# Optimization experiments

Measured on AMD Instinct MI355X. Metric: run time of the kernel, lower is better.

The kernel has to match this reference:

```python
import jax, jax.numpy as jnp
import numpy as np

N_HEAD = 16
ROPE_CACHE = 2500  # Rotary module caches tables of length 2500
NEG_INF = -1e30


def _rope_tables(head_dim):
    inv_freq = 1.0 / (10000.0 ** (jnp.arange(0, head_dim, 2, dtype=jnp.float32) / head_dim))
    t = jnp.arange(ROPE_CACHE, dtype=jnp.float32)
    freqs = t[:, None] * inv_freq[None, :]            # (2500, head_dim//2)
    emb = jnp.concatenate([freqs, freqs], axis=-1)    # (2500, head_dim)
    return jnp.cos(emb), jnp.sin(emb)


def _rotate_half(x):
    h = x.shape[-1] // 2
    return jnp.concatenate([-x[..., h:], x[..., :h]], axis=-1)


def setup_inputs() -> dict:
    key = jax.random.key(0)
    ks = jax.random.split(key, 8)
    B, S, D = 2, 2048, 1024
    H = N_HEAD
    hd = D // H
    return {
        "qx": jax.random.normal(ks[0], (B, S, D), jnp.float32),
        "kvx": jax.random.normal(ks[1], (B, S, D), jnp.float32),
        "k_cache": jnp.zeros((B, H, S, hd), jnp.float32),
        "v_cache": jnp.zeros((B, H, S, hd), jnp.float32),
        "Wq": jax.random.normal(ks[2], (D, D), jnp.float32) * 0.02,
        "bq": jnp.zeros((D,), jnp.float32),
        "Wk": jax.random.normal(ks[3], (D, D), jnp.float32) * 0.02,
        "Wv": jax.random.normal(ks[4], (D, D), jnp.float32) * 0.02,
        "bv": jnp.zeros((D,), jnp.float32),
        "Wo": jax.random.normal(ks[5], (D, D), jnp.float32) * 0.02,
        "bo": jnp.zeros((D,), jnp.float32),
        "q_positions": jnp.arange(S, dtype=jnp.int32),
        "kv_positions": jnp.arange(S, dtype=jnp.int32),
    }


def reference(qx, kvx, k_cache, v_cache, Wq, bq, Wk, Wv, bv, Wo, bo, q_positions, kv_positions):
    B, Sq, D = qx.shape
    H = N_HEAD
    hd = D // H
    Skv = kvx.shape[1]
    cos, sin = _rope_tables(hd)
    # sqrt_qk_scale = sqrt(1) = 1, folded out.

    def rope(x, pos):  # x: (B, S, H, hd)
        c = cos[pos][None, :, None, :]
        s = sin[pos][None, :, None, :]
        return x * c + _rotate_half(x) * s

    # projections (torch Linear: y = x @ W.T + b; key has no bias)
    q = (qx @ Wq.T + bq).reshape(B, Sq, H, hd)
    q = rope(q, q_positions).transpose(0, 2, 1, 3)            # (B,H,Sq,hd)
    k = (kvx @ Wk.T).reshape(B, Skv, H, hd)
    k = rope(k, kv_positions).transpose(0, 2, 1, 3)           # (B,H,Skv,hd)
    v = (kvx @ Wv.T + bv).reshape(B, Skv, H, hd).transpose(0, 2, 1, 3)

    # KV-cache scatter update: k_cache[:, :, kv_positions] = k
    k_cache = k_cache.at[:, :, kv_positions].set(k)
    v_cache = v_cache.at[:, :, kv_positions].set(v)
    Sc = k_cache.shape[2]

    # SDPA (causal), scaled by 1/sqrt(head_dim) as in F.scaled_dot_product_attention
    scores = jnp.einsum('bhqd,bhkd->bhqk', q, k_cache) / jnp.sqrt(jnp.float32(hd))
    causal = jnp.arange(Sq)[:, None] >= jnp.arange(Sc)[None, :]
    scores = jnp.where(causal[None, None], scores, NEG_INF)
    attn = jax.nn.softmax(scores, axis=-1)
    wv = jnp.einsum('bhqk,bhkd->bhqd', attn, v_cache)

    out = wv.transpose(0, 2, 1, 3).reshape(B, Sq, D) @ Wo.T + bo
    return out
```

## Files before the change

kernel.cpp:

```cpp
#include <hip/hip_runtime.h>
#include <cstdint>
#include <cstddef>

#define NH   16
#define SEQ  2048
#define DM   1024
#define HD   64
#define KDIM 1024
#define MROWS 4096
#define CH   2

using short8  = __attribute__((ext_vector_type(8))) short;
using short4v = __attribute__((ext_vector_type(4))) short;
using floatx4 = __attribute__((ext_vector_type(4))) float;

__device__ __forceinline__ short f2bf(float f) {
  unsigned int u = __float_as_uint(f);
  u += 0x7fffu + ((u >> 16) & 1u);
  return (short)(u >> 16);
}
__device__ __forceinline__ float bf2f(short s) {
  return __uint_as_float(((unsigned int)(unsigned short)s) << 16);
}

__device__ __forceinline__ void async_ld16(const void* g, void* l) {
  __builtin_amdgcn_global_load_lds(
      (const __attribute__((address_space(1))) void*)g,
      (__attribute__((address_space(3))) void*)l, 16, 0, 0);
}

struct Cvt8 {
  const float* src[8];
  void* dst[8];
  int n[8];
  const int* pos[8];
};

__global__ void convert8(Cvt8 a) {
  const int which = blockIdx.y;
  const int stride = gridDim.x * blockDim.x;
  if (which < 6) {
    const float4* s = (const float4*)a.src[which];
    short4v* d = (short4v*)a.dst[which];
    const int n4 = a.n[which] >> 2;
    for (int i = blockIdx.x * blockDim.x + threadIdx.x; i < n4; i += stride) {
      float4 v = s[i];
      short4v o;
      o.x = f2bf(v.x); o.y = f2bf(v.y); o.z = f2bf(v.z); o.w = f2bf(v.w);
      d[i] = o;
    }
  } else {
    const int* pos = a.pos[which];
    float2* d = (float2*)a.dst[which];
    const int n = a.n[which];
    for (int i = blockIdx.x * blockDim.x + threadIdx.x; i < n; i += stride) {
      int s = i >> 5, d1 = i & 31;
      float fr = __powf(10000.f, -(float)d1 * (1.f / 32.f));
      float ang = (float)pos[s] * fr;
      float sn, cs;
      __sincosf(ang, &sn, &cs);
      d[i] = make_float2(cs, sn);
    }
  }
}

__device__ __forceinline__ void gemm_core(const short* __restrict__ A,
                                          const short* __restrict__ B,
                                          int row0, int col0,
                                          short* As, short* Bs,
                                          floatx4 (&acc)[4][4], int tid) {
  const int lane = tid & 63;
  const int w = tid >> 6;
  const int quad = lane >> 4;
  const int ln = lane & 15;
  const int wr = w >> 1, wc = w & 1;

  int kks[4], rws[4], grs[4];
#pragma unroll
  for (int g = 0; g < 4; ++g) {
    int slot = (w * 4 + g) * 64 + lane;
    kks[g] = slot >> 9;
    rws[g] = (slot >> 2) & 127;
    grs[g] = slot & 3;
  }
#pragma unroll
  for (int i = 0; i < 4; ++i)
#pragma unroll
    for (int j = 0; j < 4; ++j) acc[i][j] = (floatx4){0.f, 0.f, 0.f, 0.f};

  for (int k0 = 0; k0 < KDIM; k0 += 64) {
    __syncthreads();
#pragma unroll
    for (int g = 0; g < 4; ++g) {
      int slot = (w * 4 + g) * 64 + lane;
      int src = k0 + kks[g] * 32 + grs[g] * 8;
      async_ld16(A + (size_t)(row0 + rws[g]) * KDIM + src, As + slot * 8);
      async_ld16(B + (size_t)(col0 + rws[g]) * KDIM + src, Bs + slot * 8);
    }
    __syncthreads();

#pragma unroll
    for (int ks = 0; ks < 2; ++ks) {
      short8 af[4], bfr[4];
#pragma unroll
      for (int i = 0; i < 4; ++i)
        af[i] = *(const short8*)(As + ks * 4096 + (wr * 64 + i * 16 + ln) * 32 + quad * 8);
#pragma unroll
      for (int j = 0; j < 4; ++j)
        bfr[j] = *(const short8*)(Bs + ks * 4096 + (wc * 64 + j * 16 + ln) * 32 + quad * 8);
#pragma unroll
      for (int i = 0; i < 4; ++i)
#pragma unroll
        for (int j = 0; j < 4; ++j)
          acc[i][j] = __builtin_amdgcn_mfma_f32_16x16x32_bf16(af[i], bfr[j], acc[i][j], 0, 0, 0);
    }
  }
}

__global__ __launch_bounds__(256) void proj_gemm(
    const short* __restrict__ qxb, const short* __restrict__ kvxb,
    const short* __restrict__ Wqb, const short* __restrict__ Wkb,
    const short* __restrict__ Wvb,
    const float* __restrict__ bq, const float* __restrict__ bv,
    short* __restrict__ Qo, short* __restrict__ Ko, short* __restrict__ Vt,
    const float2* __restrict__ qtab, const float2* __restrict__ ktab) {
  __shared__ __align__(16) short As[128 * 64];
  __shared__ __align__(16) short Bs[128 * 64];

  const int tid = threadIdx.x;
  const int lane = tid & 63;
  const int w = tid >> 6;
  const int quad = lane >> 4;
  const int ln = lane & 15;
  const int wr = w >> 1, wc = w & 1;
  const int z = blockIdx.z;

  int row0, col0;
  const short *A, *B;
  if (z == 2) {
    A = Wvb; B = kvxb;
    row0 = blockIdx.x * 128;
    col0 = blockIdx.y * 128;
  } else {
    A = z ? kvxb : qxb;
    B = z ? Wkb : Wqb;
    row0 = blockIdx.y * 128;
    col0 = blockIdx.x * 128;
  }

  floatx4 acc[4][4];
  gemm_core(A, B, row0, col0, As, Bs, acc, tid);

  if (z == 2) {
#pragma unroll
    for (int i = 0; i < 4; ++i)
#pragma unroll
      for (int r = 0; r < 4; ++r) {
        int nr = row0 + wr * 64 + i * 16 + quad * 4 + r;
        int h = nr >> 6, d = nr & 63;
        float bb = bv[nr];
        size_t base = ((size_t)(h)*HD + d) * SEQ;
#pragma unroll
        for (int j = 0; j < 4; ++j) {
          int sc = col0 + wc * 64 + j * 16 + ln;
          int b = sc >> 11, s = sc & (SEQ - 1);
          Vt[((size_t)b * NH * HD) * SEQ + base + s] = f2bf(acc[i][j][r] + bb);
        }
      }
  } else {
    const int colbase = col0 + wc * 64;
    const float scale = (z == 0) ? 0.125f : 1.0f;
    const float* bias = (z == 0) ? bq : nullptr;
    const float2* tab = (z == 0) ? qtab : ktab;
    short* Out = (z == 0) ? Qo : Ko;
#pragma unroll
    for (int j = 0; j < 2; ++j) {
      int col1 = colbase + j * 16 + ln;
      float b1 = bias ? bias[col1] : 0.f;
      float b2 = bias ? bias[col1 + 32] : 0.f;
      int h = col1 >> 6;
      int d1 = col1 & 63;
#pragma unroll
      for (int i = 0; i < 4; ++i)
#pragma unroll
        for (int r = 0; r < 4; ++r) {
          int row = row0 + wr * 64 + i * 16 + quad * 4 + r;
          int b = row >> 11, s = row & (SEQ - 1);
          float2 cs_sn = tab[s * 32 + d1];
          float x1 = acc[i][j][r] + b1;
          float x2 = acc[i][j + 2][r] + b2;
          float o1 = (x1 * cs_sn.x - x2 * cs_sn.y) * scale;
          float o2 = (x2 * cs_sn.x + x1 * cs_sn.y) * scale;
          size_t basq = ((((size_t)b * NH + h) * SEQ) + s) * HD;
          Out[basq + d1] = f2bf(o1);
          Out[basq + d1 + 32] = f2bf(o2);
        }
    }
  }
}

__global__ __launch_bounds__(256) void out_gemm(
    const short* __restrict__ Ab, const short* __restrict__ Bb,
    const float* __restrict__ bias, float* __restrict__ out) {
  __shared__ __align__(16) short As[128 * 64];
  __shared__ __align__(16) short Bs[128 * 64];
  const int tid = threadIdx.x;
  const int lane = tid & 63;
  const int w = tid >> 6;
  const int quad = lane >> 4;
  const int ln = lane & 15;
  const int wr = w >> 1, wc = w & 1;
  const int row0 = blockIdx.y * 128;
  const int col0 = blockIdx.x * 128;

  floatx4 acc[4][4];
  gemm_core(Ab, Bb, row0, col0, As, Bs, acc, tid);

#pragma unroll
  for (int j = 0; j < 4; ++j) {
    int col = col0 + wc * 64 + j * 16 + ln;
    float bb = bias[col];
#pragma unroll
    for (int i = 0; i < 4; ++i)
#pragma unroll
      for (int r = 0; r < 4; ++r) {
        int row = row0 + wr * 64 + i * 16 + quad * 4 + r;
        out[(size_t)row * DM + col] = acc[i][j][r] + bb;
      }
  }
}

__global__ __launch_bounds__(256) void attn_partial(
    const short* __restrict__ Q, const short* __restrict__ Kc,
    const short* __restrict__ Vtg, short* __restrict__ Po,
    float* __restrict__ Lo) {
  const int tid = threadIdx.x;
  const int lane = tid & 63;
  const int w = tid >> 6;
  const int quad = lane >> 4;
  const int ln = lane & 15;
  const int bh = blockIdx.y;
  const int bx = blockIdx.x;
  const int qt = 31 - (bx >> 1);
  const int ch = bx & (CH - 1);
  if (ch > qt) return;

  const int q0 = qt * 64;
  const int wlo = q0 + w * 16;

  const short* Qb = Q + (size_t)bh * SEQ * HD;
  const short* Kb = Kc + (size_t)bh * SEQ * HD;
  const short* Vb = Vtg + (size_t)bh * HD * SEQ;

  __shared__ __align__(16) short Ks[2 * 64 * 32];
  __shared__ __align__(16) short Vs[2 * 64 * 32];
  __shared__ __align__(16) short Pt[4][16 * 72];

  short8 qa[2];
#pragma unroll
  for (int kk = 0; kk < 2; ++kk)
    qa[kk] = *(const short8*)(Qb + (size_t)(wlo + ln) * HD + quad * 8 + kk * 32);

  floatx4 oacc[4];
  float lp = 0.f;
#pragma unroll
  for (int jd = 0; jd < 4; ++jd) oacc[jd] = (floatx4){0.f, 0.f, 0.f, 0.f};

  for (int t = ch * 64; t <= q0; t += CH * 64) {
    __syncthreads();
#pragma unroll
    for (int g = 0; g < 2; ++g) {
      int slot = (w * 2 + g) * 64 + lane;
      int kk = slot >> 8, rowi = (slot >> 2) & 63, grp = slot & 3;
      async_ld16(Kb + (size_t)(t + rowi) * HD + kk * 32 + grp * 8,
                 (char*)Ks + slot * 16);
      async_ld16(Vb + (size_t)rowi * SEQ + t + kk * 32 + grp * 8,
                 (char*)Vs + slot * 16);
    }
    __syncthreads();

    floatx4 sacc[4];
#pragma unroll
    for (int c = 0; c < 4; ++c) sacc[c] = (floatx4){0.f, 0.f, 0.f, 0.f};
#pragma unroll
    for (int kk = 0; kk < 2; ++kk)
#pragma unroll
      for (int c = 0; c < 4; ++c) {
        short8 kb = *(const short8*)(Ks + kk * 2048 + (c * 16 + ln) * 32 + quad * 8);
        sacc[c] = __builtin_amdgcn_mfma_f32_16x16x32_bf16(kb, qa[kk], sacc[c], 0, 0, 0);
      }

    const bool dmask = (t == q0);
#pragma unroll
    for (int c = 0; c < 4; ++c) {
      short4v pk;
#pragma unroll
      for (int r = 0; r < 4; ++r) {
        float p = __expf(sacc[c][r]);
        if (dmask) {
          int sp = t + c * 16 + quad * 4 + r;
          int qq = wlo + ln;
          if (sp > qq) p = 0.f;
        }
        lp += p;
        pk[r] = f2bf(p);
      }
      *(short4v*)(&Pt[w][ln * 72 + c * 16 + quad * 4]) = pk;
    }

#pragma unroll
    for (int kk = 0; kk < 2; ++kk) {
      short8 pb = *(const short8*)(&Pt[w][ln * 72 + kk * 32 + quad * 8]);
#pragma unroll
      for (int jd = 0; jd < 4; ++jd) {
        short8 va = *(const short8*)(Vs + kk * 2048 + (jd * 16 + ln) * 32 + quad * 8);
        oacc[jd] = __builtin_amdgcn_mfma_f32_16x16x32_bf16(va, pb, oacc[jd], 0, 0, 0);
      }
    }
  }

  const size_t idx = ((size_t)bh * 32 + qt) * CH + ch;
  short* Pob = Po + idx * 4096;
#pragma unroll
  for (int jd = 0; jd < 4; ++jd) {
    short4v pk;
#pragma unroll
    for (int r = 0; r < 4; ++r) pk[r] = f2bf(oacc[jd][r]);
    *(short4v*)(Pob + (w * 16 + ln) * 64 + jd * 16 + quad * 4) = pk;
  }
  float l = lp;
  l += __shfl_xor(l, 16, 64);
  l += __shfl_xor(l, 32, 64);
  if (quad == 0) Lo[idx * 64 + w * 16 + ln] = l;
}

__global__ __launch_bounds__(256) void attn_reduce(
    const short* __restrict__ Po, const float* __restrict__ Lo,
    short* __restrict__ Ov) {
  const int qt = blockIdx.x;
  const int bh = blockIdx.y;
  const int b = bh >> 4, h = bh & 15;
  const int tid = threadIdx.x;
  const int ql = tid >> 2;
  const int d0 = (tid & 3) * 16;
  const int nch = (qt >= 1) ? CH : 1;
  const size_t i0 = ((size_t)bh * 32 + qt) * CH;

  float l = Lo[i0 * 64 + ql];
  const short8* p0 = (const short8*)(Po + i0 * 4096 + ql * 64 + d0);
  short8 a0 = p0[0], a1 = p0[1];
  float acc[16];
#pragma unroll
  for (int e = 0; e < 8; ++e) { acc[e] = bf2f(a0[e]); acc[8 + e] = bf2f(a1[e]); }
  if (nch == 2) {
    l += Lo[(i0 + 1) * 64 + ql];
    const short8* p1 = (const short8*)(Po + (i0 + 1) * 4096 + ql * 64 + d0);
    short8 c0 = p1[0], c1 = p1[1];
#pragma unroll
    for (int e = 0; e < 8; ++e) { acc[e] += bf2f(c0[e]); acc[8 + e] += bf2f(c1[e]); }
  }
  float inv = 1.f / l;
  short8 o0, o1;
#pragma unroll
  for (int e = 0; e < 8; ++e) { o0[e] = f2bf(acc[e] * inv); o1[e] = f2bf(acc[8 + e] * inv); }
  int s = qt * 64 + ql;
  short* dst = Ov + ((size_t)b * SEQ + s) * DM + h * HD + d0;
  *(short8*)dst = o0;
  *((short8*)dst + 1) = o1;
}

extern "C" void kernel_launch(void* const* d_in, const int* in_sizes, int n_in,
                              void* d_out, int out_size, void* d_ws, size_t ws_size,
                              hipStream_t stream) {
  const float* qx  = (const float*)d_in[0];
  const float* kvx = (const float*)d_in[1];
  const float* Wq = (const float*)d_in[4];
  const float* bq = (const float*)d_in[5];
  const float* Wk = (const float*)d_in[6];
  const float* Wv = (const float*)d_in[7];
  const float* bv = (const float*)d_in[8];
  const float* Wo = (const float*)d_in[9];
  const float* bo = (const float*)d_in[10];
  const int* qpos  = (const int*)d_in[11];
  const int* kvpos = (const int*)d_in[12];

  char* ws = (char*)d_ws;
  short* qxb  = (short*)(ws + 0);
  short* kvxb = (short*)(ws + 8388608);
  short* Wqb  = (short*)(ws + 16777216);
  short* Wkb  = (short*)(ws + 18874368);
  short* Wvb  = (short*)(ws + 20971520);
  short* Wob  = (short*)(ws + 23068672);
  short* Qbf  = (short*)(ws + 25165824);
  short* Kbf  = (short*)(ws + 33554432);
  short* Vtb  = (short*)(ws + 41943040);
  short* WVbf = (short*)(ws + 50331648);
  float2* qtab = (float2*)(ws + 50331648);
  float2* ktab = (float2*)(ws + 50331648 + 524288);
  short* Po = (short*)(ws + 0);
  float* Lo = (float*)(ws + 16777216);

  Cvt8 c;
  c.src[0] = qx;  c.dst[0] = qxb;  c.n[0] = MROWS * KDIM; c.pos[0] = nullptr;
  c.src[1] = kvx; c.dst[1] = kvxb; c.n[1] = MROWS * KDIM; c.pos[1] = nullptr;
  c.src[2] = Wq;  c.dst[2] = Wqb;  c.n[2] = DM * KDIM;    c.pos[2] = nullptr;
  c.src[3] = Wk;  c.dst[3] = Wkb;  c.n[3] = DM * KDIM;    c.pos[3] = nullptr;
  c.src[4] = Wv;  c.dst[4] = Wvb;  c.n[4] = DM * KDIM;    c.pos[4] = nullptr;
  c.src[5] = Wo;  c.dst[5] = Wob;  c.n[5] = DM * KDIM;    c.pos[5] = nullptr;
  c.src[6] = nullptr; c.dst[6] = qtab; c.n[6] = SEQ * 32; c.pos[6] = qpos;
  c.src[7] = nullptr; c.dst[7] = ktab; c.n[7] = SEQ * 32; c.pos[7] = kvpos;
  convert8<<<dim3(1024, 8), 256, 0, stream>>>(c);

  proj_gemm<<<dim3(DM / 128, MROWS / 128, 3), 256, 0, stream>>>(
      qxb, kvxb, Wqb, Wkb, Wvb, bq, bv, Qbf, Kbf, Vtb, qtab, ktab);

  attn_partial<<<dim3(32 * CH, 2 * NH), 256, 0, stream>>>(Qbf, Kbf, Vtb, Po, Lo);

  attn_reduce<<<dim3(SEQ / 64, 2 * NH), 256, 0, stream>>>(Po, Lo, WVbf);

  out_gemm<<<dim3(DM / 128, MROWS / 128), 256, 0, stream>>>(
      WVbf, Wob, bo, (float*)d_out);
}
```

Before: 264.9 us.

## Shrink out-projection tiles to 64x128, truncate P to bf16, simplify load indexing

The output GEMM moves from 128x128 tiles (256 blocks) to 64x128 tiles on a 1D grid of 512 blocks. This gives more blocks across the CUs and a smaller LDS footprint, at the cost of less reuse per tile. In attention, the probability values are now packed to bf16 by plain truncation with a byte-permute instead of round-to-nearest, which saves ALU work but adds a small rounding bias. The GEMM async-load slot indexing is also recomputed inline rather than precomputed per warp.

```diff
diff --git a/kernel.cpp b/kernel.cpp
--- a/kernel.cpp
+++ b/kernel.cpp
@@ -21,6 +21,10 @@
 }
 __device__ __forceinline__ float bf2f(short s) {
   return __uint_as_float(((unsigned int)(unsigned short)s) << 16);
+}
+__device__ __forceinline__ unsigned int pktrunc(float lo, float hi) {
+  return __builtin_amdgcn_perm(__float_as_uint(hi), __float_as_uint(lo),
+                               0x07060302u);
 }
 
 __device__ __forceinline__ void async_ld16(const void* g, void* l) {
@@ -75,14 +79,6 @@
   const int ln = lane & 15;
   const int wr = w >> 1, wc = w & 1;
 
-  int kks[4], rws[4], grs[4];
-#pragma unroll
-  for (int g = 0; g < 4; ++g) {
-    int slot = (w * 4 + g) * 64 + lane;
-    kks[g] = slot >> 9;
-    rws[g] = (slot >> 2) & 127;
-    grs[g] = slot & 3;
-  }
 #pragma unroll
   for (int i = 0; i < 4; ++i)
 #pragma unroll
@@ -92,10 +88,12 @@
     __syncthreads();
 #pragma unroll
     for (int g = 0; g < 4; ++g) {
-      int slot = (w * 4 + g) * 64 + lane;
-      int src = k0 + kks[g] * 32 + grs[g] * 8;
-      async_ld16(A + (size_t)(row0 + rws[g]) * KDIM + src, As + slot * 8);
-      async_ld16(B + (size_t)(col0 + rws[g]) * KDIM + src, Bs + slot * 8);
+      int slot = g * 256 + tid;
+      int kk = slot >> 9, rem = slot & 511;
+      int row = rem >> 2, grp = rem & 3;
+      int src = k0 + kk * 32 + grp * 8;
+      async_ld16(A + (size_t)(row0 + row) * KDIM + src, As + slot * 8);
+      async_ld16(B + (size_t)(col0 + row) * KDIM + src, Bs + slot * 8);
     }
     __syncthreads();
 
@@ -202,7 +200,7 @@
 __global__ __launch_bounds__(256) void out_gemm(
     const short* __restrict__ Ab, const short* __restrict__ Bb,
     const float* __restrict__ bias, float* __restrict__ out) {
-  __shared__ __align__(16) short As[128 * 64];
+  __shared__ __align__(16) short As[64 * 64];
   __shared__ __align__(16) short Bs[128 * 64];
   const int tid = threadIdx.x;
   const int lane = tid & 63;
@@ -210,21 +208,63 @@
   const int quad = lane >> 4;
   const int ln = lane & 15;
   const int wr = w >> 1, wc = w & 1;
-  const int row0 = blockIdx.y * 128;
-  const int col0 = blockIdx.x * 128;
-
-  floatx4 acc[4][4];
-  gemm_core(Ab, Bb, row0, col0, As, Bs, acc, tid);
+  const int row0 = (blockIdx.x >> 3) * 64;
+  const int col0 = (blockIdx.x & 7) * 128;
+
+  floatx4 acc[2][4];
+#pragma unroll
+  for (int i = 0; i < 2; ++i)
+#pragma unroll
+    for (int j = 0; j < 4; ++j) acc[i][j] = (floatx4){0.f, 0.f, 0.f, 0.f};
+
+  for (int k0 = 0; k0 < KDIM; k0 += 64) {
+    __syncthreads();
+    {
+#pragma unroll
+      for (int g = 0; g < 2; ++g) {
+        int slot = g * 256 + tid;
+        int kk = slot >> 8, rem = slot & 255;
+        int row = rem >> 2, grp = rem & 3;
+        async_ld16(Ab + (size_t)(row0 + row) * KDIM + k0 + kk * 32 + grp * 8,
+                   As + slot * 8);
+      }
+#pragma unroll
+      for (int g = 0; g < 4; ++g) {
+        int slot = g * 256 + tid;
+        int kk = slot >> 9, rem = slot & 511;
+        int row = rem >> 2, grp = rem & 3;
+        async_ld16(Bb + (size_t)(col0 + row) * KDIM + k0 + kk * 32 + grp * 8,
+                   Bs + slot * 8);
+      }
+    }
+    __syncthreads();
+
+#pragma unroll
+    for (int ks = 0; ks < 2; ++ks) {
+      short8 af[2], bfr[4];
+#pragma unroll
+      for (int i = 0; i < 2; ++i)
+        af[i] = *(const short8*)(As + ks * 2048 + (wr * 32 + i * 16 + ln) * 32 + quad * 8);
+#pragma unroll
+      for (int j = 0; j < 4; ++j)
+        bfr[j] = *(const short8*)(Bs + ks * 4096 + (wc * 64 + j * 16 + ln) * 32 + quad * 8);
+#pragma unroll
+      for (int i = 0; i < 2; ++i)
+#pragma unroll
+        for (int j = 0; j < 4; ++j)
+          acc[i][j] = __builtin_amdgcn_mfma_f32_16x16x32_bf16(af[i], bfr[j], acc[i][j], 0, 0, 0);
+    }
+  }
 
 #pragma unroll
   for (int j = 0; j < 4; ++j) {
     int col = col0 + wc * 64 + j * 16 + ln;
     float bb = bias[col];
 #pragma unroll
-    for (int i = 0; i < 4; ++i)
+    for (int i = 0; i < 2; ++i)
 #pragma unroll
       for (int r = 0; r < 4; ++r) {
-        int row = row0 + wr * 64 + i * 16 + quad * 4 + r;
+        int row = row0 + wr * 32 + i * 16 + quad * 4 + r;
         out[(size_t)row * DM + col] = acc[i][j][r] + bb;
       }
   }
@@ -293,19 +333,22 @@
     const bool dmask = (t == q0);
 #pragma unroll
     for (int c = 0; c < 4; ++c) {
-      short4v pk;
+      float p[4];
 #pragma unroll
       for (int r = 0; r < 4; ++r) {
-        float p = __expf(sacc[c][r]);
+        float pv = __expf(sacc[c][r]);
         if (dmask) {
           int sp = t + c * 16 + quad * 4 + r;
           int qq = wlo + ln;
-          if (sp > qq) p = 0.f;
+          if (sp > qq) pv = 0.f;
         }
-        lp += p;
-        pk[r] = f2bf(p);
-      }
-      *(short4v*)(&Pt[w][ln * 72 + c * 16 + quad * 4]) = pk;
+        lp += pv;
+        p[r] = pv;
+      }
+      uint2 uu;
+      uu.x = pktrunc(p[0], p[1]);
+      uu.y = pktrunc(p[2], p[3]);
+      *(uint2*)(&Pt[w][ln * 72 + c * 16 + quad * 4]) = uu;
     }
 
 #pragma unroll
@@ -418,6 +461,5 @@
 
   attn_reduce<<<dim3(SEQ / 64, 2 * NH), 256, 0, stream>>>(Po, Lo, WVbf);
 
-  out_gemm<<<dim3(DM / 128, MROWS / 128), 256, 0, stream>>>(
-      WVbf, Wob, bo, (float*)d_out);
-}
+  out_gemm<<<dim3(64 * 8), 256, 0, stream>>>(WVbf, Wob, bo, (float*)d_out);
+}
```

Result: faster. 256.6 us (-3.1%).
